# Kernel optimization log

Hardware: AMD Instinct MI355X
Metric: run time of the kernel (lower is better)

The kernel has to match this reference:

```python
import jax, jax.numpy as jnp
import numpy as np

NEG_BIG = -9.0e15  # matches torch's -9000000000000000.0 mask fill
ALPHA = 0.2        # LeakyReLU negative slope


def setup_inputs() -> dict:
    key = jax.random.key(0)
    k1, k2, k3, k4 = jax.random.split(key, 4)
    bs, N, F_in, F_out = 4, 4096, 512, 64
    x = jax.random.normal(k1, (bs, N, F_in), dtype=jnp.float32)
    adj = jax.random.randint(k2, (N, N), 0, 2, dtype=jnp.int32)
    # xavier_uniform with gain=1.414
    lim_W = 1.414 * np.sqrt(6.0 / (F_in + F_out))
    W = jax.random.uniform(k3, (F_in, F_out), minval=-lim_W, maxval=lim_W, dtype=jnp.float32)
    lim_a = 1.414 * np.sqrt(6.0 / (2 * F_out + 1))
    a = jax.random.uniform(k4, (2 * F_out, 1), minval=-lim_a, maxval=lim_a, dtype=jnp.float32)
    return {"x": x, "adj": adj, "W": W, "a": a}


def reference(x, adj, W, a):
    # h = x @ W : [bs, N, F_out]
    h = jnp.einsum('bnf,fo->bno', x, W)
    F_out = W.shape[1]
    a1, a2 = a[:F_out, 0], a[F_out:, 0]  # each [F_out]
    # e_ij = LeakyReLU(a1.Wh_i + a2.Wh_j) -- same math as the O(N^2*2F) concat
    s1 = jnp.einsum('bno,o->bn', h, a1)  # [bs, N]
    s2 = jnp.einsum('bno,o->bn', h, a2)  # [bs, N]
    e = s1[:, :, None] + s2[:, None, :]  # [bs, N, N]
    e = jax.nn.leaky_relu(e, negative_slope=ALPHA)
    mask = (adj > 0)[None, :, :]
    attention = jnp.where(mask, e, NEG_BIG)
    attention = jax.nn.softmax(attention, axis=-1)
    # dropout is identity in eval mode (p applied only during training)
    h_prime = jnp.einsum('bij,bjo->bio', attention, h)
    return jax.nn.elu(h_prime)  # concat=True path
```

## Files before the change

### kernel.cpp

```cpp
#include <hip/hip_runtime.h>

#define LOG2E 1.4426950408889634f

typedef __attribute__((ext_vector_type(8))) short short8;
typedef __attribute__((ext_vector_type(4))) float f32x4;
using u32 = unsigned int;
using u16 = unsigned short;
using u64 = unsigned long long;

__global__ __launch_bounds__(256) void pack_mask_kernel(const int* __restrict__ adj,
                                                        u32* __restrict__ mask_t) {
    const int wid = (blockIdx.x * 256 + threadIdx.x) >> 6;
    const int lane = threadIdx.x & 63;
    for (int t = wid; t < 65536; t += 8192) {
        const int r = t >> 4, c4 = t & 15;
        const int* base = adj + (size_t)r * 4096 + c4 * 256 + lane;
        int v0 = __builtin_nontemporal_load(base);
        int v1 = __builtin_nontemporal_load(base + 64);
        int v2 = __builtin_nontemporal_load(base + 128);
        int v3 = __builtin_nontemporal_load(base + 192);
        u64 b0 = __ballot(v0 > 0);
        u64 b1 = __ballot(v1 > 0);
        u64 b2 = __ballot(v2 > 0);
        u64 b3 = __ballot(v3 > 0);
        if (lane < 8) {
            u64 bv = (lane & 4) ? ((lane & 2) ? b3 : b2) : ((lane & 2) ? b1 : b0);
            u32 w = (u32)(bv >> ((lane & 1) << 5));
            mask_t[(size_t)(c4 * 8 + lane) * 4096 + r] = w;
        }
    }
}

__global__ __launch_bounds__(256) void wt_prep(const float* __restrict__ W,
                                               u16* __restrict__ wt) {
    int t = blockIdx.x * 256 + threadIdx.x;
    int n = t >> 7, k4 = (t & 127) << 2;
    u32 c0 = __float_as_uint(W[(size_t)(k4 + 0) * 64 + n]) + 0x8000u;
    u32 c1 = __float_as_uint(W[(size_t)(k4 + 1) * 64 + n]) + 0x8000u;
    u32 c2 = __float_as_uint(W[(size_t)(k4 + 2) * 64 + n]) + 0x8000u;
    u32 c3 = __float_as_uint(W[(size_t)(k4 + 3) * 64 + n]) + 0x8000u;
    uint2 o;
    o.x = (c0 >> 16) | (c1 & 0xffff0000u);
    o.y = (c2 >> 16) | (c3 & 0xffff0000u);
    *(uint2*)(wt + (size_t)n * 512 + k4) = o;
}

__global__ __launch_bounds__(256) void k1_mfma(const float* __restrict__ x,
                                               const u16* __restrict__ wt,
                                               float* __restrict__ ph) {
    const int rt = blockIdx.x, b = blockIdx.y, kz = blockIdx.z;
    const int tid = threadIdx.x, wave = tid >> 6, lane = tid & 63;
    const int m = lane & 15, quad = lane >> 4;
    const int row = rt * 64 + wave * 16 + m;
    const float* xb = x + ((size_t)b * 4096 + row) * 512 + kz * 256 + quad * 8;
    const u16* wb = wt + (size_t)m * 512 + kz * 256 + quad * 8;

    f32x4 acc[4];
#pragma unroll
    for (int ot = 0; ot < 4; ot++) acc[ot] = (f32x4){0.f, 0.f, 0.f, 0.f};

    union BU { uint4 q; short8 v; };
    float4 ax[2][2];
    BU bw[2][4];
#pragma unroll
    for (int s = 0; s < 2; s++) {
        ax[s][0] = *(const float4*)(xb + s * 32);
        ax[s][1] = *(const float4*)(xb + s * 32 + 4);
#pragma unroll
        for (int ot = 0; ot < 4; ot++)
            bw[s][ot].q = *(const uint4*)(wb + (size_t)ot * 16 * 512 + s * 32);
    }
#pragma unroll
    for (int s = 0; s < 8; s++) {
        const int cur = s & 1;
        union { u32 u[4]; short8 v; } af;
        const float* a0 = (const float*)&ax[cur][0];
#pragma unroll
        for (int p = 0; p < 4; p++) {
            u32 lo = __float_as_uint(a0[2 * p]) + 0x8000u;
            u32 hi = __float_as_uint(a0[2 * p + 1]) + 0x8000u;
            af.u[p] = __builtin_amdgcn_perm(hi, lo, 0x07060302u);
        }
#pragma unroll
        for (int ot = 0; ot < 4; ot++)
            acc[ot] = __builtin_amdgcn_mfma_f32_16x16x32_bf16(af.v, bw[cur][ot].v,
                                                              acc[ot], 0, 0, 0);
        if (s + 2 < 8) {
            ax[cur][0] = *(const float4*)(xb + (s + 2) * 32);
            ax[cur][1] = *(const float4*)(xb + (s + 2) * 32 + 4);
#pragma unroll
            for (int ot = 0; ot < 4; ot++)
                bw[cur][ot].q =
                    *(const uint4*)(wb + (size_t)ot * 16 * 512 + (s + 2) * 32);
        }
    }
    float* pb = ph + (((size_t)(kz * 4 + b) * 4096) + rt * 64 + wave * 16) * 64;
#pragma unroll
    for (int ot = 0; ot < 4; ot++)
#pragma unroll
        for (int r = 0; r < 4; r++)
            pb[(quad * 4 + r) * 64 + ot * 16 + m] = acc[ot][r];
}

template <int KS>
__global__ __launch_bounds__(256) void k1c_fin(const float* __restrict__ ph,
                                               const float* __restrict__ a,
                                               u16* __restrict__ h_t,
                                               float* __restrict__ s1p,
                                               float* __restrict__ s2p) {
    const int b = blockIdx.y, rt = blockIdx.x;
    const int tid = threadIdx.x;
    const int rg = tid >> 4, cg = tid & 15;
    const int r0 = rg * 4, c0 = cg * 4;

    float4 v[KS][4];
#pragma unroll
    for (int s = 0; s < KS; s++) {
        const float* pb = ph + (((size_t)(s * 4 + b) * 4096) + rt * 64) * 64;
#pragma unroll
        for (int rr = 0; rr < 4; rr++)
            v[s][rr] = *(const float4*)&pb[(size_t)(r0 + rr) * 64 + c0];
    }
    float acc[4][4];
#pragma unroll
    for (int rr = 0; rr < 4; rr++) {
        acc[rr][0] = acc[rr][1] = acc[rr][2] = acc[rr][3] = 0.f;
#pragma unroll
        for (int s = 0; s < KS; s++) {
            acc[rr][0] += v[s][rr].x; acc[rr][1] += v[s][rr].y;
            acc[rr][2] += v[s][rr].z; acc[rr][3] += v[s][rr].w;
        }
    }
    float s1v[4], s2v[4];
#pragma unroll
    for (int rr = 0; rr < 4; rr++) { s1v[rr] = 0.f; s2v[rr] = 0.f; }
#pragma unroll
    for (int cc = 0; cc < 4; cc++) {
        float a1 = a[c0 + cc], a2 = a[64 + c0 + cc];
#pragma unroll
        for (int rr = 0; rr < 4; rr++) {
            s1v[rr] = fmaf(acc[rr][cc], a1, s1v[rr]);
            s2v[rr] = fmaf(acc[rr][cc], a2, s2v[rr]);
        }
    }
#pragma unroll
    for (int d = 1; d < 16; d <<= 1) {
#pragma unroll
        for (int rr = 0; rr < 4; rr++) {
            s1v[rr] += __shfl_xor(s1v[rr], d);
            s2v[rr] += __shfl_xor(s2v[rr], d);
        }
    }
    if (cg == 0) {
#pragma unroll
        for (int rr = 0; rr < 4; rr++) {
            int row = rt * 64 + r0 + rr;
            s1p[b * 4096 + row] = s1v[rr] * LOG2E;
            s2p[b * 4096 + row] = s2v[rr] * LOG2E;
        }
    }
#pragma unroll
    for (int cc = 0; cc < 4; cc++) {
        u32 b0 = __float_as_uint(acc[0][cc]) + 0x8000u;
        u32 b1 = __float_as_uint(acc[1][cc]) + 0x8000u;
        u32 b2 = __float_as_uint(acc[2][cc]) + 0x8000u;
        u32 b3 = __float_as_uint(acc[3][cc]) + 0x8000u;
        uint2 u;
        u.x = (b0 >> 16) | (b1 & 0xffff0000u);
        u.y = (b2 >> 16) | (b3 & 0xffff0000u);
        *(uint2*)(h_t + ((size_t)(b * 64 + c0 + cc)) * 4096 + rt * 64 + r0) = u;
    }
}

template <int NSTEP>
__global__ __launch_bounds__(256, 4) void k2_attn(const u16* __restrict__ h_t,
                                                  const u32* __restrict__ mask_t,
                                                  const float* __restrict__ s1p,
                                                  const float* __restrict__ s2p,
                                                  float* __restrict__ part,
                                                  float* __restrict__ lp) {
    constexpr int JSEG = NSTEP * 32;
    constexpr int T = NSTEP / 2;
    __shared__ u16 hB[2][64 * 64];
    __shared__ float s2l[JSEG];
    const int b = blockIdx.y, seg = blockIdx.z, rb = blockIdx.x;
    const int tid = threadIdx.x, wave = tid >> 6, lane = tid & 63;
    const int m = lane & 15, quad = lane >> 4;
    const int row = rb * 64 + wave * 16 + m;
    const int jstart = seg * JSEG;
    const float t1 = s1p[b * 4096 + row];
    const u16* hsrc = h_t + (size_t)b * 64 * 4096 + jstart;
    const u32* mrow = mask_t + (size_t)(jstart >> 5) * 4096 + row;

    for (int t = tid; t < (JSEG >> 2); t += 256)
        ((float4*)s2l)[t] = ((const float4*)(s2p + b * 4096 + jstart))[t];

    f32x4 acc[4], accd;
#pragma unroll
    for (int ot = 0; ot < 4; ot++) acc[ot] = (f32x4){0.f, 0.f, 0.f, 0.f};
    accd = (f32x4){0.f, 0.f, 0.f, 0.f};

    u32 mw[4];
#pragma unroll
    for (int s = 0; s < 4; s++) mw[s] = mrow[(size_t)s * 4096];
    union { u32 u[4]; short8 v; } ones;
#pragma unroll
    for (int p = 0; p < 4; p++) ones.u[p] = 0x3F803F80u;

    const int cj = tid & 7;
    const int ow = tid >> 3;
    uint4 pf[2];
    pf[0] = *(const uint4*)(hsrc + (size_t)ow * 4096 + (cj << 3));
    pf[1] = *(const uint4*)(hsrc + (size_t)(ow + 32) * 4096 + (cj << 3));
    *(uint4*)(hB[0] + (size_t)ow * 64 + ((cj ^ (ow & 7)) << 3)) = pf[0];
    *(uint4*)(hB[0] + (size_t)(ow + 32) * 64 + ((cj ^ ((ow + 32) & 7)) << 3)) = pf[1];
    __syncthreads();

    for (int jt = 0; jt < T; jt++) {
        const int cb = jt & 1;
        if (jt + 1 < T) {
            pf[0] = *(const uint4*)(hsrc + (size_t)ow * 4096 + (jt + 1) * 64 + (cj << 3));
            pf[1] = *(const uint4*)(hsrc + (size_t)(ow + 32) * 4096 + (jt + 1) * 64 + (cj << 3));
        }
#pragma unroll
        for (int ks = 0; ks < 2; ks++) {
            const int s = jt * 2 + ks;
            const u32 mws = mw[s & 3] >> (quad * 8);
            if (s + 4 < NSTEP) mw[(s + 4) & 3] = mrow[(size_t)(s + 4) * 4096];

            const float4 sa = *(const float4*)&s2l[s * 32 + quad * 8];
            const float4 sb = *(const float4*)&s2l[s * 32 + quad * 8 + 4];
            const float sv[8] = {sa.x, sa.y, sa.z, sa.w, sb.x, sb.y, sb.z, sb.w};
            union { u32 u[4]; short8 v; } af;
#pragma unroll
            for (int p = 0; p < 4; p++) {
                float t0 = t1 + sv[2 * p];
                float u0 = fmaxf(t0, 0.2f * t0);
                float w0 = __builtin_amdgcn_exp2f(u0);
                u32 m0 = (u32)(((int)(mws << (31 - 2 * p))) >> 31);
                u32 w0u = __float_as_uint(w0) & m0;
                float t2 = t1 + sv[2 * p + 1];
                float u2 = fmaxf(t2, 0.2f * t2);
                float w1 = __builtin_amdgcn_exp2f(u2);
                u32 m1 = (u32)(((int)(mws << (30 - 2 * p))) >> 31);
                u32 w1u = __float_as_uint(w1) & m1;
                af.u[p] = __builtin_amdgcn_perm(w1u, w0u, 0x07060302u);
            }
            const int jc = ks * 4 + quad;
#pragma unroll
            for (int ot = 0; ot < 4; ot++) {
                const int o = ot * 16 + m;
                short8 bfv = *(const short8*)(hB[cb] + (size_t)o * 64 + ((jc ^ (o & 7)) << 3));
                acc[ot] = __builtin_amdgcn_mfma_f32_16x16x32_bf16(af.v, bfv, acc[ot], 0, 0, 0);
            }
            accd = __builtin_amdgcn_mfma_f32_16x16x32_bf16(af.v, ones.v, accd, 0, 0, 0);
        }
        if (jt + 1 < T) {
            const int nb = cb ^ 1;
            *(uint4*)(hB[nb] + (size_t)ow * 64 + ((cj ^ (ow & 7)) << 3)) = pf[0];
            *(uint4*)(hB[nb] + (size_t)(ow + 32) * 64 + ((cj ^ ((ow + 32) & 7)) << 3)) = pf[1];
        }
        __syncthreads();
    }
    float* pb = part + (((size_t)(seg * 4 + b) * 4096) + rb * 64 + wave * 16) * 64;
#pragma unroll
    for (int ot = 0; ot < 4; ot++)
#pragma unroll
        for (int r = 0; r < 4; r++)
            pb[(quad * 4 + r) * 64 + ot * 16 + m] = acc[ot][r];
    if (m == 0) {
        float* lpb = lp + (size_t)(seg * 4 + b) * 4096 + rb * 64 + wave * 16 + quad * 4;
#pragma unroll
        for (int r = 0; r < 4; r++) lpb[r] = accd[r];
    }
}

template <int S>
__global__ __launch_bounds__(256) void k3_fin(const float* __restrict__ part,
                                              const float* __restrict__ lp,
                                              float* __restrict__ out) {
    int idx = blockIdx.x * 256 + threadIdx.x;
    int o4 = (idx & 15) << 2;
    int bi = idx >> 4;
    float4 pv[S];
    float lv[S];
#pragma unroll
    for (int s = 0; s < S; s++) {
        pv[s] = *(const float4*)&part[((size_t)s * 16384 + bi) * 64 + o4];
        lv[s] = lp[(size_t)s * 16384 + bi];
    }
    float p0 = 0.f, p1 = 0.f, p2 = 0.f, p3 = 0.f, l = 0.f;
#pragma unroll
    for (int s = 0; s < S; s++) {
        p0 += pv[s].x; p1 += pv[s].y; p2 += pv[s].z; p3 += pv[s].w;
        l += lv[s];
    }
    float rl = 1.f / l;
    p0 *= rl; p1 *= rl; p2 *= rl; p3 *= rl;
    float4 o;
    o.x = p0 > 0.f ? p0 : __builtin_amdgcn_exp2f(p0 * LOG2E) - 1.f;
    o.y = p1 > 0.f ? p1 : __builtin_amdgcn_exp2f(p1 * LOG2E) - 1.f;
    o.z = p2 > 0.f ? p2 : __builtin_amdgcn_exp2f(p2 * LOG2E) - 1.f;
    o.w = p3 > 0.f ? p3 : __builtin_amdgcn_exp2f(p3 * LOG2E) - 1.f;
    *(float4*)&out[(size_t)bi * 64 + o4] = o;
}

extern "C" void kernel_launch(void* const* d_in, const int* in_sizes, int n_in,
                              void* d_out, int out_size, void* d_ws, size_t ws_size,
                              hipStream_t stream) {
    const float* x  = (const float*)d_in[0];
    const int* adj  = (const int*)d_in[1];
    const float* W  = (const float*)d_in[2];
    const float* a  = (const float*)d_in[3];
    float* out = (float*)d_out;
    char* ws = (char*)d_ws;

    u16* h_t   = (u16*)ws;
    u32* maskt = (u32*)(ws + (2 << 20));
    float* s1p = (float*)(ws + (4 << 20));
    float* s2p = s1p + 16384;
    float* lp  = s2p + 16384;
    size_t base = (4u << 20) + 2 * 65536;
    int S = 8;
    while (S > 1 && base + (size_t)S * (65536 + 4194304) + 65536 > ws_size) S >>= 1;
    float* part = (float*)(ws + base + (size_t)S * 65536);
    u16* wtp = (u16*)(ws + base + (size_t)S * 65536 + (size_t)S * 4194304);
    const int KS = 2;

    pack_mask_kernel<<<2048, 256, 0, stream>>>(adj, maskt);
    wt_prep<<<32, 256, 0, stream>>>(W, wtp);
    k1_mfma<<<dim3(64, 4, KS), 256, 0, stream>>>(x, wtp, part);
    k1c_fin<KS><<<dim3(64, 4), 256, 0, stream>>>(part, a, h_t, s1p, s2p);
    if (S == 8)      k2_attn<16><<<dim3(64, 4, 8), 256, 0, stream>>>(h_t, maskt, s1p, s2p, part, lp);
    else if (S == 4) k2_attn<32><<<dim3(64, 4, 4), 256, 0, stream>>>(h_t, maskt, s1p, s2p, part, lp);
    else if (S == 2) k2_attn<64><<<dim3(64, 4, 2), 256, 0, stream>>>(h_t, maskt, s1p, s2p, part, lp);
    else             k2_attn<128><<<dim3(64, 4, 1), 256, 0, stream>>>(h_t, maskt, s1p, s2p, part, lp);
    if (S == 8)      k3_fin<8><<<1024, 256, 0, stream>>>(part, lp, out);
    else if (S == 4) k3_fin<4><<<1024, 256, 0, stream>>>(part, lp, out);
    else if (S == 2) k3_fin<2><<<1024, 256, 0, stream>>>(part, lp, out);
    else             k3_fin<1><<<1024, 256, 0, stream>>>(part, lp, out);
}
```

Baseline: 169.9 us.

## Fuse split-K projection with finalize via LDS reduction; reduce attention split count

```diff
diff --git a/kernel.cpp b/kernel.cpp
--- a/kernel.cpp
+++ b/kernel.cpp
@@ -45,13 +45,18 @@
     *(uint2*)(wt + (size_t)n * 512 + k4) = o;
 }
 
-__global__ __launch_bounds__(256) void k1_mfma(const float* __restrict__ x,
-                                               const u16* __restrict__ wt,
-                                               float* __restrict__ ph) {
-    const int rt = blockIdx.x, b = blockIdx.y, kz = blockIdx.z;
+__global__ __launch_bounds__(512) void k1f(const float* __restrict__ x,
+                                           const u16* __restrict__ wt,
+                                           const float* __restrict__ a,
+                                           u16* __restrict__ h_t,
+                                           float* __restrict__ s1p,
+                                           float* __restrict__ s2p) {
+    __shared__ float red[4][16][65];
+    const int rt = blockIdx.x, b = blockIdx.y;
     const int tid = threadIdx.x, wave = tid >> 6, lane = tid & 63;
+    const int g = wave & 3, kz = wave >> 2;
     const int m = lane & 15, quad = lane >> 4;
-    const int row = rt * 64 + wave * 16 + m;
+    const int row = rt * 64 + g * 16 + m;
     const float* xb = x + ((size_t)b * 4096 + row) * 512 + kz * 256 + quad * 8;
     const u16* wb = wt + (size_t)m * 512 + kz * 256 + quad * 8;
 
@@ -94,81 +99,64 @@
                     *(const uint4*)(wb + (size_t)ot * 16 * 512 + (s + 2) * 32);
         }
     }
-    float* pb = ph + (((size_t)(kz * 4 + b) * 4096) + rt * 64 + wave * 16) * 64;
+    if (kz) {
+#pragma unroll
+        for (int ot = 0; ot < 4; ot++)
+#pragma unroll
+            for (int r = 0; r < 4; r++)
+                red[g][quad * 4 + r][ot * 16 + m] = acc[ot][r];
+    }
+    __syncthreads();
+    if (kz) return;
 #pragma unroll
     for (int ot = 0; ot < 4; ot++)
 #pragma unroll
         for (int r = 0; r < 4; r++)
-            pb[(quad * 4 + r) * 64 + ot * 16 + m] = acc[ot][r];
-}
-
-template <int KS>
-__global__ __launch_bounds__(256) void k1c_fin(const float* __restrict__ ph,
-                                               const float* __restrict__ a,
-                                               u16* __restrict__ h_t,
-                                               float* __restrict__ s1p,
-                                               float* __restrict__ s2p) {
-    const int b = blockIdx.y, rt = blockIdx.x;
-    const int tid = threadIdx.x;
-    const int rg = tid >> 4, cg = tid & 15;
-    const int r0 = rg * 4, c0 = cg * 4;
-
-    float4 v[KS][4];
-#pragma unroll
-    for (int s = 0; s < KS; s++) {
-        const float* pb = ph + (((size_t)(s * 4 + b) * 4096) + rt * 64) * 64;
-#pragma unroll
-        for (int rr = 0; rr < 4; rr++)
-            v[s][rr] = *(const float4*)&pb[(size_t)(r0 + rr) * 64 + c0];
-    }
-    float acc[4][4];
-#pragma unroll
-    for (int rr = 0; rr < 4; rr++) {
-        acc[rr][0] = acc[rr][1] = acc[rr][2] = acc[rr][3] = 0.f;
-#pragma unroll
-        for (int s = 0; s < KS; s++) {
-            acc[rr][0] += v[s][rr].x; acc[rr][1] += v[s][rr].y;
-            acc[rr][2] += v[s][rr].z; acc[rr][3] += v[s][rr].w;
-        }
-    }
-    float s1v[4], s2v[4];
-#pragma unroll
-    for (int rr = 0; rr < 4; rr++) { s1v[rr] = 0.f; s2v[rr] = 0.f; }
-#pragma unroll
-    for (int cc = 0; cc < 4; cc++) {
-        float a1 = a[c0 + cc], a2 = a[64 + c0 + cc];
-#pragma unroll
-        for (int rr = 0; rr < 4; rr++) {
-            s1v[rr] = fmaf(acc[rr][cc], a1, s1v[rr]);
-            s2v[rr] = fmaf(acc[rr][cc], a2, s2v[rr]);
+            acc[ot][r] += red[g][quad * 4 + r][ot * 16 + m];
+
+    float a1v[4], a2v[4];
+#pragma unroll
+    for (int ot = 0; ot < 4; ot++) {
+        a1v[ot] = a[ot * 16 + m];
+        a2v[ot] = a[64 + ot * 16 + m];
+    }
+    float s1r[4], s2r[4];
+#pragma unroll
+    for (int r = 0; r < 4; r++) {
+        s1r[r] = 0.f; s2r[r] = 0.f;
+#pragma unroll
+        for (int ot = 0; ot < 4; ot++) {
+            s1r[r] = fmaf(acc[ot][r], a1v[ot], s1r[r]);
+            s2r[r] = fmaf(acc[ot][r], a2v[ot], s2r[r]);
         }
     }
 #pragma unroll
     for (int d = 1; d < 16; d <<= 1) {
 #pragma unroll
-        for (int rr = 0; rr < 4; rr++) {
-            s1v[rr] += __shfl_xor(s1v[rr], d);
-            s2v[rr] += __shfl_xor(s2v[rr], d);
-        }
-    }
-    if (cg == 0) {
-#pragma unroll
-        for (int rr = 0; rr < 4; rr++) {
-            int row = rt * 64 + r0 + rr;
-            s1p[b * 4096 + row] = s1v[rr] * LOG2E;
-            s2p[b * 4096 + row] = s2v[rr] * LOG2E;
-        }
-    }
-#pragma unroll
-    for (int cc = 0; cc < 4; cc++) {
-        u32 b0 = __float_as_uint(acc[0][cc]) + 0x8000u;
-        u32 b1 = __float_as_uint(acc[1][cc]) + 0x8000u;
-        u32 b2 = __float_as_uint(acc[2][cc]) + 0x8000u;
-        u32 b3 = __float_as_uint(acc[3][cc]) + 0x8000u;
+        for (int r = 0; r < 4; r++) {
+            s1r[r] += __shfl_xor(s1r[r], d);
+            s2r[r] += __shfl_xor(s2r[r], d);
+        }
+    }
+    if (m == 0) {
+#pragma unroll
+        for (int r = 0; r < 4; r++) {
+            int rr = rt * 64 + g * 16 + quad * 4 + r;
+            s1p[b * 4096 + rr] = s1r[r] * LOG2E;
+            s2p[b * 4096 + rr] = s2r[r] * LOG2E;
+        }
+    }
+#pragma unroll
+    for (int ot = 0; ot < 4; ot++) {
+        u32 b0 = __float_as_uint(acc[ot][0]) + 0x8000u;
+        u32 b1 = __float_as_uint(acc[ot][1]) + 0x8000u;
+        u32 b2 = __float_as_uint(acc[ot][2]) + 0x8000u;
+        u32 b3 = __float_as_uint(acc[ot][3]) + 0x8000u;
         uint2 u;
         u.x = (b0 >> 16) | (b1 & 0xffff0000u);
         u.y = (b2 >> 16) | (b3 & 0xffff0000u);
-        *(uint2*)(h_t + ((size_t)(b * 64 + c0 + cc)) * 4096 + rt * 64 + r0) = u;
+        *(uint2*)(h_t + ((size_t)(b * 64 + ot * 16 + m)) * 4096
+                  + rt * 64 + g * 16 + quad * 4) = u;
     }
 }
 
@@ -321,22 +309,18 @@
     float* s2p = s1p + 16384;
     float* lp  = s2p + 16384;
     size_t base = (4u << 20) + 2 * 65536;
-    int S = 8;
+    int S = 4;
     while (S > 1 && base + (size_t)S * (65536 + 4194304) + 65536 > ws_size) S >>= 1;
     float* part = (float*)(ws + base + (size_t)S * 65536);
     u16* wtp = (u16*)(ws + base + (size_t)S * 65536 + (size_t)S * 4194304);
-    const int KS = 2;
 
     pack_mask_kernel<<<2048, 256, 0, stream>>>(adj, maskt);
     wt_prep<<<32, 256, 0, stream>>>(W, wtp);
-    k1_mfma<<<dim3(64, 4, KS), 256, 0, stream>>>(x, wtp, part);
-    k1c_fin<KS><<<dim3(64, 4), 256, 0, stream>>>(part, a, h_t, s1p, s2p);
-    if (S == 8)      k2_attn<16><<<dim3(64, 4, 8), 256, 0, stream>>>(h_t, maskt, s1p, s2p, part, lp);
-    else if (S == 4) k2_attn<32><<<dim3(64, 4, 4), 256, 0, stream>>>(h_t, maskt, s1p, s2p, part, lp);
+    k1f<<<dim3(64, 4), 512, 0, stream>>>(x, wtp, a, h_t, s1p, s2p);
+    if (S == 4)      k2_attn<32><<<dim3(64, 4, 4), 256, 0, stream>>>(h_t, maskt, s1p, s2p, part, lp);
     else if (S == 2) k2_attn<64><<<dim3(64, 4, 2), 256, 0, stream>>>(h_t, maskt, s1p, s2p, part, lp);
     else             k2_attn<128><<<dim3(64, 4, 1), 256, 0, stream>>>(h_t, maskt, s1p, s2p, part, lp);
-    if (S == 8)      k3_fin<8><<<1024, 256, 0, stream>>>(part, lp, out);
-    else if (S == 4) k3_fin<4><<<1024, 256, 0, stream>>>(part, lp, out);
+    if (S == 4)      k3_fin<4><<<1024, 256, 0, stream>>>(part, lp, out);
     else if (S == 2) k3_fin<2><<<1024, 256, 0, stream>>>(part, lp, out);
     else             k3_fin<1><<<1024, 256, 0, stream>>>(part, lp, out);
 }
```

Result: no change. 166.8 us (-1.8%).
